# Kernel optimization log

Measured on AMD Instinct MI355X. Metric: run time of the kernel, lower is better.

## Reference

```python
import jax, jax.numpy as jnp
import numpy as np


def setup_inputs() -> dict:
    key = jax.random.key(0)
    k1, k2 = jax.random.split(key)
    B, S, K, N = 2, 4096, 4096, 4096
    x = jax.random.randint(k1, (B, S, K), -127, 128, dtype=jnp.int32).astype(jnp.int8)
    weight = jax.random.randint(k2, (N, K), -127, 128, dtype=jnp.int32).astype(jnp.int8)
    bias = jnp.zeros((1, N), dtype=jnp.int8)
    a = jnp.float32(0.01)   # alpha = input_scale * weight_scale / output_scale
    b = jnp.float32(1.0)    # beta = bias_scale / output_scale
    return {"x": x, "weight": weight, "bias": bias, "a": a, "b": b}


def reference(x, weight, bias, a, b):
    # i8gemm.linear_a8_w8_b8_o8: int8 GEMM with int32 accumulation, then
    # y_int8 = saturate_cast(round(alpha * acc + beta * bias)).
    x_shape = x.shape
    xf = x.reshape(-1, x_shape[-1])                     # [M, K] int8
    acc = jnp.matmul(xf, weight.T, preferred_element_type=jnp.int32)  # [M, N]
    y = a * acc.astype(jnp.float32) + b * bias.astype(jnp.float32)    # fused epilogue
    yq = jnp.clip(jnp.round(y), -128.0, 127.0).astype(jnp.int8)       # requantize o8
    return yq.reshape(*x_shape[:-1], -1)
```

## Files before the change

### kernel.cpp

```cpp
#include <hip/hip_runtime.h>
#include <stdint.h>

#define M_DIM 8192
#define N_DIM 4096
#define K_DIM 4096

using int4v = __attribute__((ext_vector_type(4))) int;

__global__ __launch_bounds__(256) void pack_kernel(const int4* __restrict__ sx,
                                                   const int4* __restrict__ sw,
                                                   unsigned int* __restrict__ dst,
                                                   int nx, int ntot) {
    int idx = blockIdx.x * blockDim.x + threadIdx.x;
    if (idx >= ntot) return;
    int4 v = (idx < nx) ? sx[idx] : sw[idx - nx];
    dst[idx] = (v.x & 0xff) | ((v.y & 0xff) << 8) | ((v.z & 0xff) << 16) |
               ((v.w & 0xff) << 24);
}

__device__ __forceinline__ void async_copy16(const char* g, char* l) {
    __builtin_amdgcn_global_load_lds(
        (const __attribute__((address_space(1))) char*)g,
        (__attribute__((address_space(3))) char*)l, 16, 0, 0);
}

__global__ __launch_bounds__(256, 2) void gemm_i8_kernel(
    const char* __restrict__ Aq,
    const char* __restrict__ Bq,
    const int* __restrict__ bias,
    const float* __restrict__ a_ptr,
    const float* __restrict__ b_ptr,
    int32_t* __restrict__ out)
{
    __shared__ char As[2][128 * 64];
    __shared__ char Bs[2][128 * 64];

    const int tid  = threadIdx.x;
    const int lane = tid & 63;
    const int wave = tid >> 6;
    const int wr   = wave >> 1;
    const int wc   = wave & 1;
    const int m0   = blockIdx.y * 128;
    const int n0   = blockIdx.x * 128;

    const float alpha = *a_ptr;
    const float beta  = *b_ptr;

    int4v acc[4][4] = {};

    const int srow = tid >> 2;
    const int scol = (tid & 3) * 16;

    const char* aG0 = Aq + (size_t)(m0 + srow) * K_DIM + scol;
    const char* aG1 = aG0 + (size_t)64 * K_DIM;
    const char* bG0 = Bq + (size_t)(n0 + srow) * K_DIM + scol;
    const char* bG1 = bG0 + (size_t)64 * K_DIM;
    const int l0 = tid * 16;
    const int l1 = tid * 16 + 4096;

    const int fr = lane & 15;
    const int fk = (lane >> 4) * 16;

    async_copy16(aG0, &As[0][l0]);
    async_copy16(aG1, &As[0][l1]);
    async_copy16(bG0, &Bs[0][l0]);
    async_copy16(bG1, &Bs[0][l1]);

    int cur = 0;
    for (int k0 = 0; k0 < K_DIM; k0 += 64) {
        __syncthreads();

        const int nxt = cur ^ 1;
        if (k0 + 64 < K_DIM) {
            async_copy16(aG0 + k0 + 64, &As[nxt][l0]);
            async_copy16(aG1 + k0 + 64, &As[nxt][l1]);
            async_copy16(bG0 + k0 + 64, &Bs[nxt][l0]);
            async_copy16(bG1 + k0 + 64, &Bs[nxt][l1]);
        }

        int4v af[4], bf[4];
#pragma unroll
        for (int i = 0; i < 4; ++i)
            af[i] = *(const int4v*)&As[cur][(wr * 64 + i * 16 + fr) * 64 + fk];
#pragma unroll
        for (int j = 0; j < 4; ++j)
            bf[j] = *(const int4v*)&Bs[cur][(wc * 64 + j * 16 + fr) * 64 + fk];

#pragma unroll
        for (int i = 0; i < 4; ++i)
#pragma unroll
            for (int j = 0; j < 4; ++j)
                acc[i][j] = __builtin_amdgcn_mfma_i32_16x16x64_i8(
                    af[i], bf[j], acc[i][j], 0, 0, 0);

        cur = nxt;
    }

    const int orow = (lane >> 4) * 4;
    const int ocol = lane & 15;
#pragma unroll
    for (int j = 0; j < 4; ++j) {
        const int gn = n0 + wc * 64 + j * 16 + ocol;
        const float bb = beta * (float)bias[gn];
#pragma unroll
        for (int i = 0; i < 4; ++i) {
            const int gm = m0 + wr * 64 + i * 16 + orow;
#pragma unroll
            for (int r = 0; r < 4; ++r) {
                float v = alpha * (float)acc[i][j][r] + bb;
                v = rintf(v);
                v = fminf(fmaxf(v, -128.0f), 127.0f);
                out[(size_t)(gm + r) * N_DIM + gn] = (int32_t)v;
            }
        }
    }
}

extern "C" void kernel_launch(void* const* d_in, const int* in_sizes, int n_in,
                              void* d_out, int out_size, void* d_ws, size_t ws_size,
                              hipStream_t stream) {
    const int*   x    = (const int*)d_in[0];
    const int*   w    = (const int*)d_in[1];
    const int*   bias = (const int*)d_in[2];
    const float* a    = (const float*)d_in[3];
    const float* b    = (const float*)d_in[4];
    int32_t*     out  = (int32_t*)d_out;

    char* xq = (char*)d_ws;
    const int nx   = (M_DIM * K_DIM) / 4;
    const int nw   = (N_DIM * K_DIM) / 4;
    const int ntot = nx + nw;
    pack_kernel<<<(ntot + 255) / 256, 256, 0, stream>>>(
        (const int4*)x, (const int4*)w, (unsigned int*)xq, nx, ntot);

    char* wq = xq + (size_t)M_DIM * K_DIM;

    dim3 grid(N_DIM / 128, M_DIM / 128);
    gemm_i8_kernel<<<grid, 256, 0, stream>>>(xq, wq, bias, a, b, out);
}
```

Before: 409.2 us.

## Swizzle LDS tile layout and drop double buffering to single buffer

Applies an XOR swizzle to the 16-byte column groups of each row, on both the global-to-LDS copy side and the fragment read side, so MFMA fragment reads spread across LDS banks instead of conflicting. It also replaces the double-buffered LDS pipeline with a single buffer, loading each K tile and then synchronizing twice per iteration. That halves LDS use, which may allow more resident blocks, but the loads for the next tile no longer overlap the current MFMAs.

```diff
diff --git a/kernel.cpp b/kernel.cpp
--- a/kernel.cpp
+++ b/kernel.cpp
@@ -32,8 +32,8 @@
     const float* __restrict__ b_ptr,
     int32_t* __restrict__ out)
 {
-    __shared__ char As[2][128 * 64];
-    __shared__ char Bs[2][128 * 64];
+    __shared__ char As[128 * 64];
+    __shared__ char Bs[128 * 64];
 
     const int tid  = threadIdx.x;
     const int lane = tid & 63;
@@ -49,42 +49,36 @@
     int4v acc[4][4] = {};
 
     const int srow = tid >> 2;
-    const int scol = (tid & 3) * 16;
+    const int sg   = (tid & 3) ^ ((srow >> 1) & 3);
+    const int scol = sg * 16;
 
     const char* aG0 = Aq + (size_t)(m0 + srow) * K_DIM + scol;
     const char* aG1 = aG0 + (size_t)64 * K_DIM;
     const char* bG0 = Bq + (size_t)(n0 + srow) * K_DIM + scol;
     const char* bG1 = bG0 + (size_t)64 * K_DIM;
-    const int l0 = tid * 16;
-    const int l1 = tid * 16 + 4096;
+    char* aL0 = &As[tid * 16];
+    char* aL1 = &As[tid * 16 + 4096];
+    char* bL0 = &Bs[tid * 16];
+    char* bL1 = &Bs[tid * 16 + 4096];
 
-    const int fr = lane & 15;
-    const int fk = (lane >> 4) * 16;
+    const int fr  = lane & 15;
+    const int gw  = lane >> 4;
+    const int fko = (gw ^ ((fr >> 1) & 3)) * 16;
 
-    async_copy16(aG0, &As[0][l0]);
-    async_copy16(aG1, &As[0][l1]);
-    async_copy16(bG0, &Bs[0][l0]);
-    async_copy16(bG1, &Bs[0][l1]);
-
-    int cur = 0;
     for (int k0 = 0; k0 < K_DIM; k0 += 64) {
+        async_copy16(aG0 + k0, aL0);
+        async_copy16(aG1 + k0, aL1);
+        async_copy16(bG0 + k0, bL0);
+        async_copy16(bG1 + k0, bL1);
         __syncthreads();
-
-        const int nxt = cur ^ 1;
-        if (k0 + 64 < K_DIM) {
-            async_copy16(aG0 + k0 + 64, &As[nxt][l0]);
-            async_copy16(aG1 + k0 + 64, &As[nxt][l1]);
-            async_copy16(bG0 + k0 + 64, &Bs[nxt][l0]);
-            async_copy16(bG1 + k0 + 64, &Bs[nxt][l1]);
-        }
 
         int4v af[4], bf[4];
 #pragma unroll
         for (int i = 0; i < 4; ++i)
-            af[i] = *(const int4v*)&As[cur][(wr * 64 + i * 16 + fr) * 64 + fk];
+            af[i] = *(const int4v*)&As[(wr * 64 + i * 16 + fr) * 64 + fko];
 #pragma unroll
         for (int j = 0; j < 4; ++j)
-            bf[j] = *(const int4v*)&Bs[cur][(wc * 64 + j * 16 + fr) * 64 + fk];
+            bf[j] = *(const int4v*)&Bs[(wc * 64 + j * 16 + fr) * 64 + fko];
 
 #pragma unroll
         for (int i = 0; i < 4; ++i)
@@ -93,7 +87,7 @@
                 acc[i][j] = __builtin_amdgcn_mfma_i32_16x16x64_i8(
                     af[i], bf[j], acc[i][j], 0, 0, 0);
 
-        cur = nxt;
+        __syncthreads();
     }
 
     const int orow = (lane >> 4) * 4;
```

After: 416.3 us. About the same (+1.7%).

## Replace async LDS loads with register-staged prefetch and XOR-swizzled LDS layout

Applied to the files above, without the earlier changes.

Drops global_load_lds direct-to-LDS copies in favour of a register-staged pipeline. Global loads for tile k+2 are issued into registers while tile k is computed, and tile k+1 is written to the other LDS buffer. The LDS column chunk is XOR-swizzled by row so fragment reads avoid bank conflicts. This costs more VGPRs, which may limit occupancy under the two-blocks-per-CU bound, and adds a VGPR-to-LDS write step on each iteration.

```diff
diff --git a/kernel.cpp b/kernel.cpp
--- a/kernel.cpp
+++ b/kernel.cpp
@@ -16,12 +16,6 @@
     int4 v = (idx < nx) ? sx[idx] : sw[idx - nx];
     dst[idx] = (v.x & 0xff) | ((v.y & 0xff) << 8) | ((v.z & 0xff) << 16) |
                ((v.w & 0xff) << 24);
-}
-
-__device__ __forceinline__ void async_copy16(const char* g, char* l) {
-    __builtin_amdgcn_global_load_lds(
-        (const __attribute__((address_space(1))) char*)g,
-        (__attribute__((address_space(3))) char*)l, 16, 0, 0);
 }
 
 __global__ __launch_bounds__(256, 2) void gemm_i8_kernel(
@@ -49,7 +43,7 @@
     int4v acc[4][4] = {};
 
     const int srow = tid >> 2;
-    const int scol = (tid & 3) * 16;
+    const int scol = ((tid & 3) ^ ((srow >> 1) & 3)) * 16;
 
     const char* aG0 = Aq + (size_t)(m0 + srow) * K_DIM + scol;
     const char* aG1 = aG0 + (size_t)64 * K_DIM;
@@ -58,33 +52,49 @@
     const int l0 = tid * 16;
     const int l1 = tid * 16 + 4096;
 
-    const int fr = lane & 15;
-    const int fk = (lane >> 4) * 16;
+    const int fr  = lane & 15;
+    const int gw  = lane >> 4;
+    const int fko = (gw ^ ((fr >> 1) & 3)) * 16;
 
-    async_copy16(aG0, &As[0][l0]);
-    async_copy16(aG1, &As[0][l1]);
-    async_copy16(bG0, &Bs[0][l0]);
-    async_copy16(bG1, &Bs[0][l1]);
+    int4v ra0 = *(const int4v*)aG0;
+    int4v ra1 = *(const int4v*)aG1;
+    int4v rb0 = *(const int4v*)bG0;
+    int4v rb1 = *(const int4v*)bG1;
+    *(int4v*)&As[0][l0] = ra0;
+    *(int4v*)&As[0][l1] = ra1;
+    *(int4v*)&Bs[0][l0] = rb0;
+    *(int4v*)&Bs[0][l1] = rb1;
+    ra0 = *(const int4v*)(aG0 + 64);
+    ra1 = *(const int4v*)(aG1 + 64);
+    rb0 = *(const int4v*)(bG0 + 64);
+    rb1 = *(const int4v*)(bG1 + 64);
+    __syncthreads();
 
-    int cur = 0;
+#pragma unroll 2
     for (int k0 = 0; k0 < K_DIM; k0 += 64) {
-        __syncthreads();
+        const int cur = (k0 >> 6) & 1;
+        const int nxt = cur ^ 1;
 
-        const int nxt = cur ^ 1;
         if (k0 + 64 < K_DIM) {
-            async_copy16(aG0 + k0 + 64, &As[nxt][l0]);
-            async_copy16(aG1 + k0 + 64, &As[nxt][l1]);
-            async_copy16(bG0 + k0 + 64, &Bs[nxt][l0]);
-            async_copy16(bG1 + k0 + 64, &Bs[nxt][l1]);
+            *(int4v*)&As[nxt][l0] = ra0;
+            *(int4v*)&As[nxt][l1] = ra1;
+            *(int4v*)&Bs[nxt][l0] = rb0;
+            *(int4v*)&Bs[nxt][l1] = rb1;
+        }
+        if (k0 + 128 < K_DIM) {
+            ra0 = *(const int4v*)(aG0 + k0 + 128);
+            ra1 = *(const int4v*)(aG1 + k0 + 128);
+            rb0 = *(const int4v*)(bG0 + k0 + 128);
+            rb1 = *(const int4v*)(bG1 + k0 + 128);
         }
 
         int4v af[4], bf[4];
 #pragma unroll
         for (int i = 0; i < 4; ++i)
-            af[i] = *(const int4v*)&As[cur][(wr * 64 + i * 16 + fr) * 64 + fk];
+            af[i] = *(const int4v*)&As[cur][(wr * 64 + i * 16 + fr) * 64 + fko];
 #pragma unroll
         for (int j = 0; j < 4; ++j)
-            bf[j] = *(const int4v*)&Bs[cur][(wc * 64 + j * 16 + fr) * 64 + fk];
+            bf[j] = *(const int4v*)&Bs[cur][(wc * 64 + j * 16 + fr) * 64 + fko];
 
 #pragma unroll
         for (int i = 0; i < 4; ++i)
@@ -93,7 +103,7 @@
                 acc[i][j] = __builtin_amdgcn_mfma_i32_16x16x64_i8(
                     af[i], bf[j], acc[i][j], 0, 0, 0);
 
-        cur = nxt;
+        __syncthreads();
     }
 
     const int orow = (lane >> 4) * 4;
```

Measured after the change: 413.7 us. No clear change (+1.1%).

## Load MFMA fragments directly from global into registers, dropping LDS staging

Applied to the files above, without the earlier changes.

Removes the shared-memory tiles and async global-to-LDS copies. Each wave now loads its A and B MFMA fragments directly from global memory into registers, software-pipelined two K-steps deep. This eliminates the block-wide barrier each iteration and raises the occupancy hint to 3 blocks. In exchange, waves no longer share tiles, so global/L2 traffic doubles and loads are less coalesced.

```diff
diff --git a/kernel.cpp b/kernel.cpp
--- a/kernel.cpp
+++ b/kernel.cpp
@@ -18,13 +18,7 @@
                ((v.w & 0xff) << 24);
 }
 
-__device__ __forceinline__ void async_copy16(const char* g, char* l) {
-    __builtin_amdgcn_global_load_lds(
-        (const __attribute__((address_space(1))) char*)g,
-        (__attribute__((address_space(3))) char*)l, 16, 0, 0);
-}
-
-__global__ __launch_bounds__(256, 2) void gemm_i8_kernel(
+__global__ __launch_bounds__(256, 3) void gemm_i8_kernel(
     const char* __restrict__ Aq,
     const char* __restrict__ Bq,
     const int* __restrict__ bias,
@@ -32,9 +26,6 @@
     const float* __restrict__ b_ptr,
     int32_t* __restrict__ out)
 {
-    __shared__ char As[2][128 * 64];
-    __shared__ char Bs[2][128 * 64];
-
     const int tid  = threadIdx.x;
     const int lane = tid & 63;
     const int wave = tid >> 6;
@@ -48,52 +39,46 @@
 
     int4v acc[4][4] = {};
 
-    const int srow = tid >> 2;
-    const int scol = (tid & 3) * 16;
-
-    const char* aG0 = Aq + (size_t)(m0 + srow) * K_DIM + scol;
-    const char* aG1 = aG0 + (size_t)64 * K_DIM;
-    const char* bG0 = Bq + (size_t)(n0 + srow) * K_DIM + scol;
-    const char* bG1 = bG0 + (size_t)64 * K_DIM;
-    const int l0 = tid * 16;
-    const int l1 = tid * 16 + 4096;
-
     const int fr = lane & 15;
     const int fk = (lane >> 4) * 16;
+    const char* aRow = Aq + (size_t)(m0 + wr * 64 + fr) * K_DIM + fk;
+    const char* bRow = Bq + (size_t)(n0 + wc * 64 + fr) * K_DIM + fk;
+    const size_t rstep = (size_t)16 * K_DIM;
 
-    async_copy16(aG0, &As[0][l0]);
-    async_copy16(aG1, &As[0][l1]);
-    async_copy16(bG0, &Bs[0][l0]);
-    async_copy16(bG1, &Bs[0][l1]);
+    int4v af0[4], bf0[4], af1[4], bf1[4];
 
-    int cur = 0;
-    for (int k0 = 0; k0 < K_DIM; k0 += 64) {
-        __syncthreads();
+#pragma unroll
+    for (int i = 0; i < 4; ++i) {
+        af0[i] = *(const int4v*)(aRow + (size_t)i * rstep);
+        bf0[i] = *(const int4v*)(bRow + (size_t)i * rstep);
+    }
 
-        const int nxt = cur ^ 1;
-        if (k0 + 64 < K_DIM) {
-            async_copy16(aG0 + k0 + 64, &As[nxt][l0]);
-            async_copy16(aG1 + k0 + 64, &As[nxt][l1]);
-            async_copy16(bG0 + k0 + 64, &Bs[nxt][l0]);
-            async_copy16(bG1 + k0 + 64, &Bs[nxt][l1]);
+    for (int k0 = 0; k0 < K_DIM; k0 += 128) {
+#pragma unroll
+        for (int i = 0; i < 4; ++i) {
+            af1[i] = *(const int4v*)(aRow + (size_t)i * rstep + k0 + 64);
+            bf1[i] = *(const int4v*)(bRow + (size_t)i * rstep + k0 + 64);
         }
-
-        int4v af[4], bf[4];
-#pragma unroll
-        for (int i = 0; i < 4; ++i)
-            af[i] = *(const int4v*)&As[cur][(wr * 64 + i * 16 + fr) * 64 + fk];
-#pragma unroll
-        for (int j = 0; j < 4; ++j)
-            bf[j] = *(const int4v*)&Bs[cur][(wc * 64 + j * 16 + fr) * 64 + fk];
-
 #pragma unroll
         for (int i = 0; i < 4; ++i)
 #pragma unroll
             for (int j = 0; j < 4; ++j)
                 acc[i][j] = __builtin_amdgcn_mfma_i32_16x16x64_i8(
-                    af[i], bf[j], acc[i][j], 0, 0, 0);
+                    af0[i], bf0[j], acc[i][j], 0, 0, 0);
 
-        cur = nxt;
+        if (k0 + 128 < K_DIM) {
+#pragma unroll
+            for (int i = 0; i < 4; ++i) {
+                af0[i] = *(const int4v*)(aRow + (size_t)i * rstep + k0 + 128);
+                bf0[i] = *(const int4v*)(bRow + (size_t)i * rstep + k0 + 128);
+            }
+        }
+#pragma unroll
+        for (int i = 0; i < 4; ++i)
+#pragma unroll
+            for (int j = 0; j < 4; ++j)
+                acc[i][j] = __builtin_amdgcn_mfma_i32_16x16x64_i8(
+                    af1[i], bf1[j], acc[i][j], 0, 0, 0);
     }
 
     const int orow = (lane >> 4) * 4;
```

Result: slower. 709.4 us (+73.4%).
